# Kernel optimization log

Hardware: AMD Instinct MI355X
Metric: run time of the kernel (lower is better)

## Reference

```python
import jax, jax.numpy as jnp
import numpy as np

N = 100000      # num vertices
E = 20000       # num hyperedges
NNZ = 600000    # num incidence pairs
D = 128         # feature dim (in_features == out_features)


def _scatter_mean(src, idx, num_segments):
    # mean-reduce rows of src into num_segments buckets; empty buckets -> 0 (matches torch_scatter mean)
    s = jax.ops.segment_sum(src, idx, num_segments=num_segments)
    cnt = jax.ops.segment_sum(jnp.ones((src.shape[0], 1), src.dtype), idx, num_segments=num_segments)
    return s / jnp.maximum(cnt, 1)


def setup_inputs() -> dict:
    key = jax.random.key(0)
    k1, k2, k3, k4, k5 = jax.random.split(key, 5)
    X = jax.random.normal(k1, (N, D), dtype=jnp.float32)
    X0 = jax.random.normal(k2, (N, D), dtype=jnp.float32)
    # nn.Linear weight: [out_features, in_features], kaiming-uniform-ish scale
    W = jax.random.normal(k3, (D, D), dtype=jnp.float32) / np.float32(np.sqrt(D))
    vertex = jax.random.randint(k4, (NNZ,), 0, N)
    edges = jax.random.randint(k5, (NNZ,), 0, E)
    alpha = jnp.float32(0.1)
    beta = jnp.float32(0.5)
    return {"X": X, "vertex": vertex, "edges": edges, "alpha": alpha, "beta": beta, "X0": X0, "W": W}


def reference(X, vertex, edges, alpha, beta, X0, W):
    # vertex -> hyperedge gather + mean
    Xve = X[vertex]                                   # [NNZ, D]
    Xe = _scatter_mean(Xve, edges, E)                 # [E, D]
    # hyperedge -> vertex gather + mean
    Xev = Xe[edges]                                   # [NNZ, D]
    Xv = _scatter_mean(Xev, vertex, N)                # [N, D]
    # GCNII residual mixing (UniGNN_use_norm=False)
    Xi = (1.0 - alpha) * Xv + alpha * X0
    return (1.0 - beta) * Xi + beta * (Xi @ W.T)
```

## Files before the change

kernel.cpp:

```cpp
#include <hip/hip_runtime.h>

#define NV   100000
#define NE   20000
#define NNZP 600000
#define DIM  128
#define SE   80
#define SV   32

#define NB_E 79
#define NB_V 98
#define CAP_E 8448
#define CAP_V 6912
#define BIN_BLOCKS ((NNZP / 8 + 255) / 256)
#define G_CVT1 256
#define G_CVT2 384
#define XSPLIT4 1280000
#define EDGE_BLOCKS (NE * 16 / 256)

typedef __attribute__((ext_vector_type(8))) short short8;
typedef __attribute__((ext_vector_type(4))) float f32x4;

__device__ __forceinline__ unsigned short f2b(float f) {
    unsigned x = __float_as_uint(f);
    unsigned r = x + 0x7fffu + ((x >> 16) & 1u);
    return (unsigned short)(r >> 16);
}
__device__ __forceinline__ float blo(unsigned u) { return __uint_as_float(u << 16); }
__device__ __forceinline__ float bhi(unsigned u) { return __uint_as_float(u & 0xffff0000u); }
__device__ __forceinline__ unsigned pk2(float a, float b) {
    return (unsigned)f2b(a) | ((unsigned)f2b(b) << 16);
}

__global__ __launch_bounds__(256) void k_bin(const float4* __restrict__ X4,
                                             const float4* __restrict__ W4,
                                             const float* __restrict__ beta_p,
                                             const int4* __restrict__ vertex4,
                                             const int4* __restrict__ edges4,
                                             unsigned* __restrict__ gpos_e,
                                             unsigned* __restrict__ gpos_v,
                                             unsigned* __restrict__ ebin,
                                             unsigned* __restrict__ vbin,
                                             ushort4* __restrict__ Xb,
                                             ushort4* __restrict__ Mb) {
    const int b = blockIdx.x;
    if (b >= BIN_BLOCKS) {
        int i = (b - BIN_BLOCKS) * 256 + threadIdx.x;
        for (int g = i; g < XSPLIT4; g += G_CVT1 * 256) {
            float4 v = X4[g];
            ushort4 o; o.x = f2b(v.x); o.y = f2b(v.y); o.z = f2b(v.z); o.w = f2b(v.w);
            Xb[g] = o;
        }
        if (i < DIM * DIM / 4) {
            const float beta = *beta_p;
            const float omb  = 1.0f - beta;
            float4 v = W4[i];
            int c  = i >> 5;
            int k0 = (i & 31) * 4;
            ushort4 o;
            o.x = f2b(beta * v.x + ((k0 + 0) == c ? omb : 0.f));
            o.y = f2b(beta * v.y + ((k0 + 1) == c ? omb : 0.f));
            o.z = f2b(beta * v.z + ((k0 + 2) == c ? omb : 0.f));
            o.w = f2b(beta * v.w + ((k0 + 3) == c ? omb : 0.f));
            Mb[i] = o;
        }
        return;
    }

    __shared__ unsigned he[NB_E], hv[NB_V], be[NB_E], bv[NB_V];
    const int tid = threadIdx.x;
    if (tid < NB_E) he[tid] = 0;
    if (tid < NB_V) hv[tid] = 0;
    __syncthreads();

    const int t8 = b * 256 + tid;
    const bool ok = t8 < NNZP / 8;
    int vA[8], eA[8];
    unsigned loe[8], lov[8];
    if (ok) {
        int4 v0 = vertex4[t8 * 2], v1 = vertex4[t8 * 2 + 1];
        int4 e0 = edges4[t8 * 2],  e1 = edges4[t8 * 2 + 1];
        vA[0]=v0.x; vA[1]=v0.y; vA[2]=v0.z; vA[3]=v0.w;
        vA[4]=v1.x; vA[5]=v1.y; vA[6]=v1.z; vA[7]=v1.w;
        eA[0]=e0.x; eA[1]=e0.y; eA[2]=e0.z; eA[3]=e0.w;
        eA[4]=e1.x; eA[5]=e1.y; eA[6]=e1.z; eA[7]=e1.w;
#pragma unroll
        for (int k = 0; k < 8; ++k) {
            loe[k] = atomicAdd(&he[eA[k] >> 8], 1u);
            lov[k] = atomicAdd(&hv[vA[k] >> 10], 1u);
        }
    }
    __syncthreads();

    for (int i = tid; i < NB_E; i += 256) {
        int bin = (i + b) % NB_E;
        unsigned h = he[bin];
        be[bin] = h ? atomicAdd(&gpos_e[bin], h) : 0u;
    }
    for (int i = tid; i < NB_V; i += 256) {
        int bin = (i + b) % NB_V;
        unsigned h = hv[bin];
        bv[bin] = h ? atomicAdd(&gpos_v[bin], h) : 0u;
    }
    __syncthreads();

    if (ok) {
#pragma unroll
        for (int k = 0; k < 8; ++k) {
            unsigned e = (unsigned)eA[k], v = (unsigned)vA[k];
            unsigned binE = e >> 8, binV = v >> 10;
            unsigned pe = be[binE] + loe[k];
            if (pe < CAP_E) ebin[(size_t)binE * CAP_E + pe] = (v << 8) | (e & 255u);
            unsigned pv = bv[binV] + lov[k];
            if (pv < CAP_V) vbin[(size_t)binV * CAP_V + pv] = (e << 10) | (v & 1023u);
        }
    }
}

__global__ __launch_bounds__(256) void k_bucket(const unsigned* __restrict__ gpos_e,
                                                const unsigned* __restrict__ gpos_v,
                                                const unsigned* __restrict__ ebin,
                                                const unsigned* __restrict__ vbin,
                                                int* __restrict__ bkt_e,
                                                unsigned short* __restrict__ bkt_v,
                                                const float4* __restrict__ X4,
                                                ushort4* __restrict__ Xb) {
    const int tid = threadIdx.x;
    if (blockIdx.x >= NB_E + NB_V) {
        int i = (blockIdx.x - NB_E - NB_V) * 256 + tid;
        const int n4 = NV * 32;
        for (int g = XSPLIT4 + i; g < n4; g += G_CVT2 * 256) {
            float4 v = X4[g];
            ushort4 o; o.x = f2b(v.x); o.y = f2b(v.y); o.z = f2b(v.z); o.w = f2b(v.w);
            Xb[g] = o;
        }
        return;
    }

    __shared__ unsigned cl[1024];
    if (blockIdx.x < NB_E) {
        const int b = blockIdx.x;
        cl[tid] = 0;
        __syncthreads();
        unsigned n = gpos_e[b]; if (n > CAP_E) n = CAP_E;
        const unsigned* src = ebin + (size_t)b * CAP_E;
        for (unsigned i = tid; i < n; i += 256) {
            unsigned pk = src[i];
            unsigned el = pk & 255u;
            unsigned slot = atomicAdd(&cl[el], 1u);
            if (slot < SE - 1)
                bkt_e[(size_t)(((unsigned)b << 8) | el) * SE + 1 + slot] = (int)(pk >> 8);
        }
        __syncthreads();
        int e = (b << 8) | tid;
        if (e < NE) bkt_e[(size_t)e * SE] = (int)cl[tid];
    } else {
        const int b = blockIdx.x - NB_E;
        for (int i = tid; i < 1024; i += 256) cl[i] = 0;
        __syncthreads();
        unsigned n = gpos_v[b]; if (n > CAP_V) n = CAP_V;
        const unsigned* src = vbin + (size_t)b * CAP_V;
        for (unsigned i = tid; i < n; i += 256) {
            unsigned pk = src[i];
            unsigned vl = pk & 1023u;
            unsigned slot = atomicAdd(&cl[vl], 1u);
            unsigned v = ((unsigned)b << 10) | vl;
            if (slot < SV - 1)
                bkt_v[(size_t)v * SV + 1 + slot] = (unsigned short)(pk >> 10);
        }
        __syncthreads();
        for (int i = tid; i < 1024; i += 256) {
            int v = (b << 10) + i;
            if (v < NV) bkt_v[(size_t)v * SV] = (unsigned short)cl[i];
        }
    }
}

__global__ __launch_bounds__(256) void k_edge(const uint4* __restrict__ X4b,
                                              const int4* __restrict__ bkt4,
                                              uint4* __restrict__ Xeb4) {
    const int t  = blockIdx.x * 256 + threadIdx.x;
    const int e  = t >> 4;
    const int hl = t & 15;
    const int4* bp = bkt4 + (size_t)e * (SE / 4);
    int4 q0 = bp[0], q1 = bp[1], q2 = bp[2], q3 = bp[3], q4 = bp[4], q5 = bp[5],
         q6 = bp[6], q7 = bp[7], q8 = bp[8], q9 = bp[9], q10 = bp[10];
    unsigned c = (unsigned)q0.x; if (c > SE - 1) c = SE - 1;

    float a0=0.f,a1=0.f,a2=0.f,a3=0.f,a4=0.f,a5=0.f,a6=0.f,a7=0.f;

#define EACC(g_, w_) { a0 += (w_) * blo((g_).x); a1 += (w_) * bhi((g_).x); \
                       a2 += (w_) * blo((g_).y); a3 += (w_) * bhi((g_).y); \
                       a4 += (w_) * blo((g_).z); a5 += (w_) * bhi((g_).z); \
                       a6 += (w_) * blo((g_).w); a7 += (w_) * bhi((g_).w); }
#define EG8(qa, qb, base_) { \
        int id_[8] = {(qa).x, (qa).y, (qa).z, (qa).w, (qb).x, (qb).y, (qb).z, (qb).w}; \
        float wk_[8]; uint4 g_[8]; \
        _Pragma("unroll") \
        for (int k_ = 0; k_ < 8; ++k_) { \
            bool act_ = ((base_) + k_) < c; \
            wk_[k_] = act_ ? 1.0f : 0.0f; \
            g_[k_] = X4b[(size_t)(act_ ? (unsigned)id_[k_] : 0u) * 16 + hl]; \
        } \
        _Pragma("unroll") \
        for (int k_ = 0; k_ < 8; ++k_) EACC(g_[k_], wk_[k_]); }

    {
        int id[3] = {q0.y, q0.z, q0.w};
        float wk[3]; uint4 g[3];
#pragma unroll
        for (int k = 0; k < 3; ++k) {
            bool act = (unsigned)k < c;
            wk[k] = act ? 1.0f : 0.0f;
            g[k] = X4b[(size_t)(act ? (unsigned)id[k] : 0u) * 16 + hl];
        }
#pragma unroll
        for (int k = 0; k < 3; ++k) EACC(g[k], wk[k]);
    }
    if (c > 3)  EG8(q1, q2, 3u);
    if (c > 11) EG8(q3, q4, 11u);
    if (c > 19) EG8(q5, q6, 19u);
    if (c > 27) EG8(q7, q8, 27u);
    if (c > 35) EG8(q9, q10, 35u);
    for (unsigned j = 43; j < c; j += 8) {
        int4 qa = bp[(j + 1) >> 2];
        int4 qb = bp[((j + 1) >> 2) + 1];
        EG8(qa, qb, j);
    }
#undef EG8
#undef EACC

    const float inv = c ? 1.0f / (float)c : 1.0f;
    uint4 o;
    o.x = pk2(a0 * inv, a1 * inv);
    o.y = pk2(a2 * inv, a3 * inv);
    o.z = pk2(a4 * inv, a5 * inv);
    o.w = pk2(a6 * inv, a7 * inv);
    Xeb4[(size_t)e * 16 + hl] = o;
}

__global__ __launch_bounds__(256) void k_vf2(const uint4* __restrict__ Xeb4,
                                             const uint4* __restrict__ bktq,
                                             const float4* __restrict__ X04,
                                             const float* __restrict__ alpha_p,
                                             const unsigned short* __restrict__ Mb,
                                             float* __restrict__ out) {
    __shared__ __align__(16) unsigned sXi[16][68];

    const int tid  = threadIdx.x;
    const int wid  = tid >> 6;
    const int lane = tid & 63;
    const int q    = lane >> 4;
    const int hl   = lane & 15;
    const int vrow = wid * 4 + q;
    const int v    = blockIdx.x * 16 + vrow;

    const float alpha = *alpha_p;

    float4 x0a = X04[(size_t)v * 32 + hl * 2];
    float4 x0b = X04[(size_t)v * 32 + hl * 2 + 1];

    uint4 q0 = bktq[(size_t)v * 4];
    uint4 q1 = bktq[(size_t)v * 4 + 1];
    unsigned c = q0.x & 0xffffu; if (c > SV - 1) c = SV - 1;

    float a[8] = {0.f, 0.f, 0.f, 0.f, 0.f, 0.f, 0.f, 0.f};

#define VACC(g_, w_) { a[0] += (w_) * blo((g_).x); a[1] += (w_) * bhi((g_).x); \
                       a[2] += (w_) * blo((g_).y); a[3] += (w_) * bhi((g_).y); \
                       a[4] += (w_) * blo((g_).z); a[5] += (w_) * bhi((g_).z); \
                       a[6] += (w_) * blo((g_).w); a[7] += (w_) * bhi((g_).w); }

    {
        unsigned id[7] = { q0.x >> 16, q0.y & 0xffffu, q0.y >> 16,
                           q0.z & 0xffffu, q0.z >> 16, q0.w & 0xffffu, q0.w >> 16 };
        float wk[7]; uint4 g[7];
#pragma unroll
        for (int k = 0; k < 7; ++k) {
            bool act = (unsigned)k < c;
            wk[k] = act ? 1.0f : 0.0f;
            g[k] = Xeb4[(size_t)(act ? id[k] : 0u) * 16 + hl];
        }
#pragma unroll
        for (int k = 0; k < 7; ++k) VACC(g[k], wk[k]);
    }
    if (c > 7) {
        unsigned id[8] = { q1.x & 0xffffu, q1.x >> 16, q1.y & 0xffffu, q1.y >> 16,
                           q1.z & 0xffffu, q1.z >> 16, q1.w & 0xffffu, q1.w >> 16 };
        float wk[8]; uint4 g[8];
#pragma unroll
        for (int k = 0; k < 8; ++k) {
            bool act = (unsigned)(7 + k) < c;
            wk[k] = act ? 1.0f : 0.0f;
            g[k] = Xeb4[(size_t)(act ? id[k] : 0u) * 16 + hl];
        }
#pragma unroll
        for (int k = 0; k < 8; ++k) VACC(g[k], wk[k]);
    }
    if (c > 15) {
        uint4 q2 = bktq[(size_t)v * 4 + 2];
        uint4 q3 = bktq[(size_t)v * 4 + 3];
        unsigned id[16] = { q2.x & 0xffffu, q2.x >> 16, q2.y & 0xffffu, q2.y >> 16,
                            q2.z & 0xffffu, q2.z >> 16, q2.w & 0xffffu, q2.w >> 16,
                            q3.x & 0xffffu, q3.x >> 16, q3.y & 0xffffu, q3.y >> 16,
                            q3.z & 0xffffu, q3.z >> 16, q3.w & 0xffffu, q3.w >> 16 };
        float wk[16]; uint4 g[16];
#pragma unroll
        for (int k = 0; k < 16; ++k) {
            bool act = (unsigned)(15 + k) < c;
            wk[k] = act ? 1.0f : 0.0f;
            g[k] = Xeb4[(size_t)(act ? id[k] : 0u) * 16 + hl];
        }
#pragma unroll
        for (int k = 0; k < 16; ++k) VACC(g[k], wk[k]);
    }
#undef VACC

    const float s = (1.0f - alpha) * (c ? 1.0f / (float)c : 1.0f);
    uint4 xiw;
    xiw.x = pk2(s * a[0] + alpha * x0a.x, s * a[1] + alpha * x0a.y);
    xiw.y = pk2(s * a[2] + alpha * x0a.z, s * a[3] + alpha * x0a.w);
    xiw.z = pk2(s * a[4] + alpha * x0b.x, s * a[5] + alpha * x0b.y);
    xiw.w = pk2(s * a[6] + alpha * x0b.z, s * a[7] + alpha * x0b.w);
    *(uint4*)&sXi[vrow][hl * 4] = xiw;
    __syncthreads();

    const int lr = lane & 15;
    const int lg = lane >> 4;

    const char* ab = (const char*)&sXi[lr][0] + lg * 16;
    short8 af[4];
#pragma unroll
    for (int kt = 0; kt < 4; ++kt) af[kt] = *(const short8*)(ab + kt * 64);

#pragma unroll
    for (int ctl = 0; ctl < 2; ++ctl) {
        const int ct = wid * 2 + ctl;
        const unsigned short* Wp = Mb + (size_t)(ct * 16 + lr) * DIM + lg * 8;
        f32x4 acc = {};
#pragma unroll
        for (int kt = 0; kt < 4; ++kt) {
            short8 b = *(const short8*)(Wp + kt * 32);
            acc = __builtin_amdgcn_mfma_f32_16x16x32_bf16(af[kt], b, acc, 0, 0, 0);
        }
#pragma unroll
        for (int rg = 0; rg < 4; ++rg) {
            int row = lg * 4 + rg;
            out[(size_t)(blockIdx.x * 16 + row) * DIM + ct * 16 + lr] = acc[rg];
        }
    }
}

extern "C" void kernel_launch(void* const* d_in, const int* in_sizes, int n_in,
                              void* d_out, int out_size, void* d_ws, size_t ws_size,
                              hipStream_t stream) {
    const float* X      = (const float*)d_in[0];
    const int*   vertex = (const int*)  d_in[1];
    const int*   edges  = (const int*)  d_in[2];
    const float* alpha  = (const float*)d_in[3];
    const float* beta   = (const float*)d_in[4];
    const float* X0     = (const float*)d_in[5];
    const float* W      = (const float*)d_in[6];
    float*       out    = (float*)d_out;

    unsigned* gpos_e = (unsigned*)d_ws;
    unsigned* gpos_v = gpos_e + NB_E;
    unsigned* ebin   = (unsigned*)d_ws + 256;
    unsigned* vbin   = ebin + (size_t)NB_E * CAP_E;
    int*      bkt_e  = (int*)(vbin + (size_t)NB_V * CAP_V);
    unsigned short* bkt_v = (unsigned short*)(bkt_e + (size_t)NE * SE);
    unsigned short* Mb = bkt_v + (size_t)NV * SV;
    unsigned* Xeb = (unsigned*)(Mb + DIM * DIM);

    unsigned* Xb = (unsigned*)d_out;

    hipMemsetAsync(d_ws, 0, (size_t)(NB_E + NB_V) * sizeof(unsigned), stream);

    k_bin<<<BIN_BLOCKS + G_CVT1, 256, 0, stream>>>(
        (const float4*)X, (const float4*)W, beta,
        (const int4*)vertex, (const int4*)edges,
        gpos_e, gpos_v, ebin, vbin, (ushort4*)Xb, (ushort4*)Mb);
    k_bucket<<<NB_E + NB_V + G_CVT2, 256, 0, stream>>>(
        gpos_e, gpos_v, ebin, vbin, bkt_e, bkt_v,
        (const float4*)X, (ushort4*)Xb);
    k_edge<<<EDGE_BLOCKS, 256, 0, stream>>>((const uint4*)Xb,
                                            (const int4*)bkt_e,
                                            (uint4*)Xeb);
    k_vf2<<<NV / 16, 256, 0, stream>>>((const uint4*)Xeb, (const uint4*)bkt_v,
                                       (const float4*)X0, alpha,
                                       (const unsigned short*)Mb, out);
}
```

Before: 121.8 us.

## Make vertex-finalize kernel persistent with hoisted weights and prefetched next tile

Converts k_vf2 from one 16-vertex tile per block (6250 blocks) into a grid-stride persistent kernel with 1024 blocks. Each block loads its W fragments into registers once and reuses them across tiles, and it prefetches the next tile's X0 rows and bucket headers before the MFMA stage. The aim is to cut per-block launch and weight-reload overhead and to hide load latency. In exchange it uses more registers (launch bounds of 4 waves), adds a second barrier per tile, and may load-balance worse across CUs.

New measurement: 133.4 us. 9.5% more time.

```diff
diff --git a/kernel.cpp b/kernel.cpp
--- a/kernel.cpp
+++ b/kernel.cpp
@@ -16,6 +16,8 @@
 #define G_CVT2 384
 #define XSPLIT4 1280000
 #define EDGE_BLOCKS (NE * 16 / 256)
+#define VF2_BLOCKS 1024
+#define VF2_TILES  (NV / 16)
 
 typedef __attribute__((ext_vector_type(8))) short short8;
 typedef __attribute__((ext_vector_type(4))) float f32x4;
@@ -238,12 +240,12 @@
     Xeb4[(size_t)e * 16 + hl] = o;
 }
 
-__global__ __launch_bounds__(256) void k_vf2(const uint4* __restrict__ Xeb4,
-                                             const uint4* __restrict__ bktq,
-                                             const float4* __restrict__ X04,
-                                             const float* __restrict__ alpha_p,
-                                             const unsigned short* __restrict__ Mb,
-                                             float* __restrict__ out) {
+__global__ __launch_bounds__(256, 4) void k_vf2(const uint4* __restrict__ Xeb4,
+                                                const uint4* __restrict__ bktq,
+                                                const float4* __restrict__ X04,
+                                                const float* __restrict__ alpha_p,
+                                                const unsigned short* __restrict__ Mb,
+                                                float* __restrict__ out) {
     __shared__ __align__(16) unsigned sXi[16][68];
 
     const int tid  = threadIdx.x;
@@ -252,102 +254,125 @@
     const int q    = lane >> 4;
     const int hl   = lane & 15;
     const int vrow = wid * 4 + q;
-    const int v    = blockIdx.x * 16 + vrow;
+    const int lr   = lane & 15;
+    const int lg   = lane >> 4;
 
     const float alpha = *alpha_p;
 
+    short8 mf[2][4];
+#pragma unroll
+    for (int ctl = 0; ctl < 2; ++ctl) {
+        const unsigned short* Wp = Mb + (size_t)((wid * 2 + ctl) * 16 + lr) * DIM + lg * 8;
+#pragma unroll
+        for (int kt = 0; kt < 4; ++kt)
+            mf[ctl][kt] = *(const short8*)(Wp + kt * 32);
+    }
+
+    int tile = blockIdx.x;
+    int v = tile * 16 + vrow;
     float4 x0a = X04[(size_t)v * 32 + hl * 2];
     float4 x0b = X04[(size_t)v * 32 + hl * 2 + 1];
-
     uint4 q0 = bktq[(size_t)v * 4];
     uint4 q1 = bktq[(size_t)v * 4 + 1];
-    unsigned c = q0.x & 0xffffu; if (c > SV - 1) c = SV - 1;
-
-    float a[8] = {0.f, 0.f, 0.f, 0.f, 0.f, 0.f, 0.f, 0.f};
 
 #define VACC(g_, w_) { a[0] += (w_) * blo((g_).x); a[1] += (w_) * bhi((g_).x); \
                        a[2] += (w_) * blo((g_).y); a[3] += (w_) * bhi((g_).y); \
                        a[4] += (w_) * blo((g_).z); a[5] += (w_) * bhi((g_).z); \
                        a[6] += (w_) * blo((g_).w); a[7] += (w_) * bhi((g_).w); }
 
-    {
-        unsigned id[7] = { q0.x >> 16, q0.y & 0xffffu, q0.y >> 16,
-                           q0.z & 0xffffu, q0.z >> 16, q0.w & 0xffffu, q0.w >> 16 };
-        float wk[7]; uint4 g[7];
-#pragma unroll
-        for (int k = 0; k < 7; ++k) {
-            bool act = (unsigned)k < c;
-            wk[k] = act ? 1.0f : 0.0f;
-            g[k] = Xeb4[(size_t)(act ? id[k] : 0u) * 16 + hl];
-        }
-#pragma unroll
-        for (int k = 0; k < 7; ++k) VACC(g[k], wk[k]);
-    }
-    if (c > 7) {
-        unsigned id[8] = { q1.x & 0xffffu, q1.x >> 16, q1.y & 0xffffu, q1.y >> 16,
-                           q1.z & 0xffffu, q1.z >> 16, q1.w & 0xffffu, q1.w >> 16 };
-        float wk[8]; uint4 g[8];
-#pragma unroll
-        for (int k = 0; k < 8; ++k) {
-            bool act = (unsigned)(7 + k) < c;
-            wk[k] = act ? 1.0f : 0.0f;
-            g[k] = Xeb4[(size_t)(act ? id[k] : 0u) * 16 + hl];
-        }
-#pragma unroll
-        for (int k = 0; k < 8; ++k) VACC(g[k], wk[k]);
-    }
-    if (c > 15) {
-        uint4 q2 = bktq[(size_t)v * 4 + 2];
-        uint4 q3 = bktq[(size_t)v * 4 + 3];
-        unsigned id[16] = { q2.x & 0xffffu, q2.x >> 16, q2.y & 0xffffu, q2.y >> 16,
-                            q2.z & 0xffffu, q2.z >> 16, q2.w & 0xffffu, q2.w >> 16,
-                            q3.x & 0xffffu, q3.x >> 16, q3.y & 0xffffu, q3.y >> 16,
-                            q3.z & 0xffffu, q3.z >> 16, q3.w & 0xffffu, q3.w >> 16 };
-        float wk[16]; uint4 g[16];
-#pragma unroll
-        for (int k = 0; k < 16; ++k) {
-            bool act = (unsigned)(15 + k) < c;
-            wk[k] = act ? 1.0f : 0.0f;
-            g[k] = Xeb4[(size_t)(act ? id[k] : 0u) * 16 + hl];
-        }
-#pragma unroll
-        for (int k = 0; k < 16; ++k) VACC(g[k], wk[k]);
+    while (true) {
+        unsigned c = q0.x & 0xffffu; if (c > SV - 1) c = SV - 1;
+        float a[8] = {0.f, 0.f, 0.f, 0.f, 0.f, 0.f, 0.f, 0.f};
+
+        {
+            unsigned id[7] = { q0.x >> 16, q0.y & 0xffffu, q0.y >> 16,
+                               q0.z & 0xffffu, q0.z >> 16, q0.w & 0xffffu, q0.w >> 16 };
+            float wk[7]; uint4 g[7];
+#pragma unroll
+            for (int k = 0; k < 7; ++k) {
+                bool act = (unsigned)k < c;
+                wk[k] = act ? 1.0f : 0.0f;
+                g[k] = Xeb4[(size_t)(act ? id[k] : 0u) * 16 + hl];
+            }
+#pragma unroll
+            for (int k = 0; k < 7; ++k) VACC(g[k], wk[k]);
+        }
+        if (c > 7) {
+            unsigned id[8] = { q1.x & 0xffffu, q1.x >> 16, q1.y & 0xffffu, q1.y >> 16,
+                               q1.z & 0xffffu, q1.z >> 16, q1.w & 0xffffu, q1.w >> 16 };
+            float wk[8]; uint4 g[8];
+#pragma unroll
+            for (int k = 0; k < 8; ++k) {
+                bool act = (unsigned)(7 + k) < c;
+                wk[k] = act ? 1.0f : 0.0f;
+                g[k] = Xeb4[(size_t)(act ? id[k] : 0u) * 16 + hl];
+            }
+#pragma unroll
+            for (int k = 0; k < 8; ++k) VACC(g[k], wk[k]);
+        }
+        if (c > 15) {
+            uint4 q2 = bktq[(size_t)v * 4 + 2];
+            uint4 q3 = bktq[(size_t)v * 4 + 3];
+            unsigned id[16] = { q2.x & 0xffffu, q2.x >> 16, q2.y & 0xffffu, q2.y >> 16,
+                                q2.z & 0xffffu, q2.z >> 16, q2.w & 0xffffu, q2.w >> 16,
+                                q3.x & 0xffffu, q3.x >> 16, q3.y & 0xffffu, q3.y >> 16,
+                                q3.z & 0xffffu, q3.z >> 16, q3.w & 0xffffu, q3.w >> 16 };
+            float wk[16]; uint4 g[16];
+#pragma unroll
+            for (int k = 0; k < 16; ++k) {
+                bool act = (unsigned)(15 + k) < c;
+                wk[k] = act ? 1.0f : 0.0f;
+                g[k] = Xeb4[(size_t)(act ? id[k] : 0u) * 16 + hl];
+            }
+#pragma unroll
+            for (int k = 0; k < 16; ++k) VACC(g[k], wk[k]);
+        }
+
+        const float s = (1.0f - alpha) * (c ? 1.0f / (float)c : 1.0f);
+        uint4 xiw;
+        xiw.x = pk2(s * a[0] + alpha * x0a.x, s * a[1] + alpha * x0a.y);
+        xiw.y = pk2(s * a[2] + alpha * x0a.z, s * a[3] + alpha * x0a.w);
+        xiw.z = pk2(s * a[4] + alpha * x0b.x, s * a[5] + alpha * x0b.y);
+        xiw.w = pk2(s * a[6] + alpha * x0b.z, s * a[7] + alpha * x0b.w);
+        *(uint4*)&sXi[vrow][hl * 4] = xiw;
+
+        const int ntile = tile + VF2_BLOCKS;
+        const bool more = ntile < VF2_TILES;
+        const int nv = ntile * 16 + vrow;
+        float4 nx0a, nx0b; uint4 nq0, nq1;
+        if (more) {
+            nx0a = X04[(size_t)nv * 32 + hl * 2];
+            nx0b = X04[(size_t)nv * 32 + hl * 2 + 1];
+            nq0 = bktq[(size_t)nv * 4];
+            nq1 = bktq[(size_t)nv * 4 + 1];
+        }
+        __syncthreads();
+
+        const char* ab = (const char*)&sXi[lr][0] + lg * 16;
+        short8 af[4];
+#pragma unroll
+        for (int kt = 0; kt < 4; ++kt) af[kt] = *(const short8*)(ab + kt * 64);
+
+#pragma unroll
+        for (int ctl = 0; ctl < 2; ++ctl) {
+            const int ct = wid * 2 + ctl;
+            f32x4 acc = {};
+#pragma unroll
+            for (int kt = 0; kt < 4; ++kt)
+                acc = __builtin_amdgcn_mfma_f32_16x16x32_bf16(af[kt], mf[ctl][kt], acc, 0, 0, 0);
+#pragma unroll
+            for (int rg = 0; rg < 4; ++rg) {
+                int row = lg * 4 + rg;
+                out[(size_t)(tile * 16 + row) * DIM + ct * 16 + lr] = acc[rg];
+            }
+        }
+        __syncthreads();
+
+        if (!more) break;
+        tile = ntile; v = nv;
+        x0a = nx0a; x0b = nx0b; q0 = nq0; q1 = nq1;
     }
 #undef VACC
-
-    const float s = (1.0f - alpha) * (c ? 1.0f / (float)c : 1.0f);
-    uint4 xiw;
-    xiw.x = pk2(s * a[0] + alpha * x0a.x, s * a[1] + alpha * x0a.y);
-    xiw.y = pk2(s * a[2] + alpha * x0a.z, s * a[3] + alpha * x0a.w);
-    xiw.z = pk2(s * a[4] + alpha * x0b.x, s * a[5] + alpha * x0b.y);
-    xiw.w = pk2(s * a[6] + alpha * x0b.z, s * a[7] + alpha * x0b.w);
-    *(uint4*)&sXi[vrow][hl * 4] = xiw;
-    __syncthreads();
-
-    const int lr = lane & 15;
-    const int lg = lane >> 4;
-
-    const char* ab = (const char*)&sXi[lr][0] + lg * 16;
-    short8 af[4];
-#pragma unroll
-    for (int kt = 0; kt < 4; ++kt) af[kt] = *(const short8*)(ab + kt * 64);
-
-#pragma unroll
-    for (int ctl = 0; ctl < 2; ++ctl) {
-        const int ct = wid * 2 + ctl;
-        const unsigned short* Wp = Mb + (size_t)(ct * 16 + lr) * DIM + lg * 8;
-        f32x4 acc = {};
-#pragma unroll
-        for (int kt = 0; kt < 4; ++kt) {
-            short8 b = *(const short8*)(Wp + kt * 32);
-            acc = __builtin_amdgcn_mfma_f32_16x16x32_bf16(af[kt], b, acc, 0, 0, 0);
-        }
-#pragma unroll
-        for (int rg = 0; rg < 4; ++rg) {
-            int row = lg * 4 + rg;
-            out[(size_t)(blockIdx.x * 16 + row) * DIM + ct * 16 + lr] = acc[rg];
-        }
-    }
 }
 
 extern "C" void kernel_launch(void* const* d_in, const int* in_sizes, int n_in,
@@ -385,7 +410,7 @@
     k_edge<<<EDGE_BLOCKS, 256, 0, stream>>>((const uint4*)Xb,
                                             (const int4*)bkt_e,
                                             (uint4*)Xeb);
-    k_vf2<<<NV / 16, 256, 0, stream>>>((const uint4*)Xeb, (const uint4*)bkt_v,
-                                       (const float4*)X0, alpha,
-                                       (const unsigned short*)Mb, out);
-}
+    k_vf2<<<VF2_BLOCKS, 256, 0, stream>>>((const uint4*)Xeb, (const uint4*)bkt_v,
+                                          (const float4*)X0, alpha,
+                                          (const unsigned short*)Mb, out);
+}
```

## Double-buffer edge gathers and process two vertex rows per thread in k_vf2

Applied to the files above, without the earlier changes.

In k_edge, the gather loads for each group of 8 incidences are split from their accumulation and alternated between two register buffers, so the next group's loads are issued before the previous group's FMAs. In k_vf2, each block now handles 32 vertices instead of 16. Each thread interleaves the first gathers of two vertices to raise memory-level parallelism, and reuses the W tiles loaded for the MFMA across two row tiles. Register pressure rises in both kernels and the k_vf2 grid is halved, which may lower occupancy.

New measurement: 122.4 us. No clear change (+0.5%).

```diff
diff --git a/kernel.cpp b/kernel.cpp
--- a/kernel.cpp
+++ b/kernel.cpp
@@ -16,6 +16,7 @@
 #define G_CVT2 384
 #define XSPLIT4 1280000
 #define EDGE_BLOCKS (NE * 16 / 256)
+#define VF2_BLOCKS (NV / 32)
 
 typedef __attribute__((ext_vector_type(8))) short short8;
 typedef __attribute__((ext_vector_type(4))) float f32x4;
@@ -192,41 +193,48 @@
                        a2 += (w_) * blo((g_).y); a3 += (w_) * bhi((g_).y); \
                        a4 += (w_) * blo((g_).z); a5 += (w_) * bhi((g_).z); \
                        a6 += (w_) * blo((g_).w); a7 += (w_) * bhi((g_).w); }
-#define EG8(qa, qb, base_) { \
+#define LD8(gb_, wb_, qa, qb, base_) { \
         int id_[8] = {(qa).x, (qa).y, (qa).z, (qa).w, (qb).x, (qb).y, (qb).z, (qb).w}; \
-        float wk_[8]; uint4 g_[8]; \
         _Pragma("unroll") \
         for (int k_ = 0; k_ < 8; ++k_) { \
             bool act_ = ((base_) + k_) < c; \
-            wk_[k_] = act_ ? 1.0f : 0.0f; \
-            g_[k_] = X4b[(size_t)(act_ ? (unsigned)id_[k_] : 0u) * 16 + hl]; \
-        } \
+            wb_[k_] = act_ ? 1.0f : 0.0f; \
+            gb_[k_] = X4b[(size_t)(act_ ? (unsigned)id_[k_] : 0u) * 16 + hl]; \
+        } }
+#define FM8(gb_, wb_) { \
         _Pragma("unroll") \
-        for (int k_ = 0; k_ < 8; ++k_) EACC(g_[k_], wk_[k_]); }
-
-    {
+        for (int k_ = 0; k_ < 8; ++k_) EACC(gb_[k_], wb_[k_]); }
+
+    float w0[3]; uint4 g0[3];
+#pragma unroll
+    for (int k = 0; k < 3; ++k) {
         int id[3] = {q0.y, q0.z, q0.w};
-        float wk[3]; uint4 g[3];
-#pragma unroll
-        for (int k = 0; k < 3; ++k) {
-            bool act = (unsigned)k < c;
-            wk[k] = act ? 1.0f : 0.0f;
-            g[k] = X4b[(size_t)(act ? (unsigned)id[k] : 0u) * 16 + hl];
-        }
-#pragma unroll
-        for (int k = 0; k < 3; ++k) EACC(g[k], wk[k]);
-    }
-    if (c > 3)  EG8(q1, q2, 3u);
-    if (c > 11) EG8(q3, q4, 11u);
-    if (c > 19) EG8(q5, q6, 19u);
-    if (c > 27) EG8(q7, q8, 27u);
-    if (c > 35) EG8(q9, q10, 35u);
+        bool act = (unsigned)k < c;
+        w0[k] = act ? 1.0f : 0.0f;
+        g0[k] = X4b[(size_t)(act ? (unsigned)id[k] : 0u) * 16 + hl];
+    }
+
+    float wX[8], wY[8]; uint4 gX[8], gY[8];
+    if (c > 3)  LD8(gX, wX, q1, q2, 3u);
+#pragma unroll
+    for (int k = 0; k < 3; ++k) EACC(g0[k], w0[k]);
+    if (c > 11) LD8(gY, wY, q3, q4, 11u);
+    if (c > 3)  FM8(gX, wX);
+    if (c > 19) LD8(gX, wX, q5, q6, 19u);
+    if (c > 11) FM8(gY, wY);
+    if (c > 27) LD8(gY, wY, q7, q8, 27u);
+    if (c > 19) FM8(gX, wX);
+    if (c > 35) LD8(gX, wX, q9, q10, 35u);
+    if (c > 27) FM8(gY, wY);
+    if (c > 35) FM8(gX, wX);
     for (unsigned j = 43; j < c; j += 8) {
         int4 qa = bp[(j + 1) >> 2];
         int4 qb = bp[((j + 1) >> 2) + 1];
-        EG8(qa, qb, j);
-    }
-#undef EG8
+        LD8(gY, wY, qa, qb, j);
+        FM8(gY, wY);
+    }
+#undef LD8
+#undef FM8
 #undef EACC
 
     const float inv = c ? 1.0f / (float)c : 1.0f;
@@ -244,7 +252,7 @@
                                              const float* __restrict__ alpha_p,
                                              const unsigned short* __restrict__ Mb,
                                              float* __restrict__ out) {
-    __shared__ __align__(16) unsigned sXi[16][68];
+    __shared__ __align__(16) unsigned sXi[32][68];
 
     const int tid  = threadIdx.x;
     const int wid  = tid >> 6;
@@ -252,53 +260,73 @@
     const int q    = lane >> 4;
     const int hl   = lane & 15;
     const int vrow = wid * 4 + q;
-    const int v    = blockIdx.x * 16 + vrow;
+    const int lr   = lane & 15;
+    const int lg   = lane >> 4;
 
     const float alpha = *alpha_p;
-
-    float4 x0a = X04[(size_t)v * 32 + hl * 2];
-    float4 x0b = X04[(size_t)v * 32 + hl * 2 + 1];
-
-    uint4 q0 = bktq[(size_t)v * 4];
-    uint4 q1 = bktq[(size_t)v * 4 + 1];
-    unsigned c = q0.x & 0xffffu; if (c > SV - 1) c = SV - 1;
-
-    float a[8] = {0.f, 0.f, 0.f, 0.f, 0.f, 0.f, 0.f, 0.f};
-
-#define VACC(g_, w_) { a[0] += (w_) * blo((g_).x); a[1] += (w_) * bhi((g_).x); \
-                       a[2] += (w_) * blo((g_).y); a[3] += (w_) * bhi((g_).y); \
-                       a[4] += (w_) * blo((g_).z); a[5] += (w_) * bhi((g_).z); \
-                       a[6] += (w_) * blo((g_).w); a[7] += (w_) * bhi((g_).w); }
+    const int v0 = blockIdx.x * 32 + vrow;
+    const int v1 = v0 + 16;
+
+    uint4 q0a = bktq[(size_t)v0 * 4];
+    uint4 q1a = bktq[(size_t)v0 * 4 + 1];
+    uint4 q0b = bktq[(size_t)v1 * 4];
+    uint4 q1b = bktq[(size_t)v1 * 4 + 1];
+    float4 x0a0 = X04[(size_t)v0 * 32 + hl * 2];
+    float4 x0b0 = X04[(size_t)v0 * 32 + hl * 2 + 1];
+    float4 x0a1 = X04[(size_t)v1 * 32 + hl * 2];
+    float4 x0b1 = X04[(size_t)v1 * 32 + hl * 2 + 1];
+
+    unsigned ca = q0a.x & 0xffffu; if (ca > SV - 1) ca = SV - 1;
+    unsigned cb = q0b.x & 0xffffu; if (cb > SV - 1) cb = SV - 1;
+
+    float aA[8] = {0.f,0.f,0.f,0.f,0.f,0.f,0.f,0.f};
+    float aB[8] = {0.f,0.f,0.f,0.f,0.f,0.f,0.f,0.f};
+
+#define VACC(acc_, g_, w_) { acc_[0] += (w_) * blo((g_).x); acc_[1] += (w_) * bhi((g_).x); \
+                             acc_[2] += (w_) * blo((g_).y); acc_[3] += (w_) * bhi((g_).y); \
+                             acc_[4] += (w_) * blo((g_).z); acc_[5] += (w_) * bhi((g_).z); \
+                             acc_[6] += (w_) * blo((g_).w); acc_[7] += (w_) * bhi((g_).w); }
 
     {
-        unsigned id[7] = { q0.x >> 16, q0.y & 0xffffu, q0.y >> 16,
-                           q0.z & 0xffffu, q0.z >> 16, q0.w & 0xffffu, q0.w >> 16 };
-        float wk[7]; uint4 g[7];
+        unsigned idA[7] = { q0a.x >> 16, q0a.y & 0xffffu, q0a.y >> 16,
+                            q0a.z & 0xffffu, q0a.z >> 16, q0a.w & 0xffffu, q0a.w >> 16 };
+        unsigned idB[7] = { q0b.x >> 16, q0b.y & 0xffffu, q0b.y >> 16,
+                            q0b.z & 0xffffu, q0b.z >> 16, q0b.w & 0xffffu, q0b.w >> 16 };
+        float wA[7], wB[7]; uint4 gA[7], gB[7];
 #pragma unroll
         for (int k = 0; k < 7; ++k) {
-            bool act = (unsigned)k < c;
+            bool act = (unsigned)k < ca;
+            wA[k] = act ? 1.0f : 0.0f;
+            gA[k] = Xeb4[(size_t)(act ? idA[k] : 0u) * 16 + hl];
+        }
+#pragma unroll
+        for (int k = 0; k < 7; ++k) {
+            bool act = (unsigned)k < cb;
+            wB[k] = act ? 1.0f : 0.0f;
+            gB[k] = Xeb4[(size_t)(act ? idB[k] : 0u) * 16 + hl];
+        }
+#pragma unroll
+        for (int k = 0; k < 7; ++k) VACC(aA, gA[k], wA[k]);
+#pragma unroll
+        for (int k = 0; k < 7; ++k) VACC(aB, gB[k], wB[k]);
+    }
+
+    if (ca > 7) {
+        unsigned id[8] = { q1a.x & 0xffffu, q1a.x >> 16, q1a.y & 0xffffu, q1a.y >> 16,
+                           q1a.z & 0xffffu, q1a.z >> 16, q1a.w & 0xffffu, q1a.w >> 16 };
+        float wk[8]; uint4 g[8];
+#pragma unroll
+        for (int k = 0; k < 8; ++k) {
+            bool act = (unsigned)(7 + k) < ca;
             wk[k] = act ? 1.0f : 0.0f;
             g[k] = Xeb4[(size_t)(act ? id[k] : 0u) * 16 + hl];
         }
 #pragma unroll
-        for (int k = 0; k < 7; ++k) VACC(g[k], wk[k]);
-    }
-    if (c > 7) {
-        unsigned id[8] = { q1.x & 0xffffu, q1.x >> 16, q1.y & 0xffffu, q1.y >> 16,
-                           q1.z & 0xffffu, q1.z >> 16, q1.w & 0xffffu, q1.w >> 16 };
-        float wk[8]; uint4 g[8];
-#pragma unroll
-        for (int k = 0; k < 8; ++k) {
-            bool act = (unsigned)(7 + k) < c;
-            wk[k] = act ? 1.0f : 0.0f;
-            g[k] = Xeb4[(size_t)(act ? id[k] : 0u) * 16 + hl];
-        }
-#pragma unroll
-        for (int k = 0; k < 8; ++k) VACC(g[k], wk[k]);
-    }
-    if (c > 15) {
-        uint4 q2 = bktq[(size_t)v * 4 + 2];
-        uint4 q3 = bktq[(size_t)v * 4 + 3];
+        for (int k = 0; k < 8; ++k) VACC(aA, g[k], wk[k]);
+    }
+    if (ca > 15) {
+        uint4 q2 = bktq[(size_t)v0 * 4 + 2];
+        uint4 q3 = bktq[(size_t)v0 * 4 + 3];
         unsigned id[16] = { q2.x & 0xffffu, q2.x >> 16, q2.y & 0xffffu, q2.y >> 16,
                             q2.z & 0xffffu, q2.z >> 16, q2.w & 0xffffu, q2.w >> 16,
                             q3.x & 0xffffu, q3.x >> 16, q3.y & 0xffffu, q3.y >> 16,
@@ -306,46 +334,90 @@
         float wk[16]; uint4 g[16];
 #pragma unroll
         for (int k = 0; k < 16; ++k) {
-            bool act = (unsigned)(15 + k) < c;
+            bool act = (unsigned)(15 + k) < ca;
             wk[k] = act ? 1.0f : 0.0f;
             g[k] = Xeb4[(size_t)(act ? id[k] : 0u) * 16 + hl];
         }
 #pragma unroll
-        for (int k = 0; k < 16; ++k) VACC(g[k], wk[k]);
+        for (int k = 0; k < 16; ++k) VACC(aA, g[k], wk[k]);
+    }
+
+    if (cb > 7) {
+        unsigned id[8] = { q1b.x & 0xffffu, q1b.x >> 16, q1b.y & 0xffffu, q1b.y >> 16,
+                           q1b.z & 0xffffu, q1b.z >> 16, q1b.w & 0xffffu, q1b.w >> 16 };
+        float wk[8]; uint4 g[8];
+#pragma unroll
+        for (int k = 0; k < 8; ++k) {
+            bool act = (unsigned)(7 + k) < cb;
+            wk[k] = act ? 1.0f : 0.0f;
+            g[k] = Xeb4[(size_t)(act ? id[k] : 0u) * 16 + hl];
+        }
+#pragma unroll
+        for (int k = 0; k < 8; ++k) VACC(aB, g[k], wk[k]);
+    }
+    if (cb > 15) {
+        uint4 q2 = bktq[(size_t)v1 * 4 + 2];
+        uint4 q3 = bktq[(size_t)v1 * 4 + 3];
+        unsigned id[16] = { q2.x & 0xffffu, q2.x >> 16, q2.y & 0xffffu, q2.y >> 16,
+                            q2.z & 0xffffu, q2.z >> 16, q2.w & 0xffffu, q2.w >> 16,
+                            q3.x & 0xffffu, q3.x >> 16, q3.y & 0xffffu, q3.y >> 16,
+                            q3.z & 0xffffu, q3.z >> 16, q3.w & 0xffffu, q3.w >> 16 };
+        float wk[16]; uint4 g[16];
+#pragma unroll
+        for (int k = 0; k < 16; ++k) {
+            bool act = (unsigned)(15 + k) < cb;
+            wk[k] = act ? 1.0f : 0.0f;
+            g[k] = Xeb4[(size_t)(act ? id[k] : 0u) * 16 + hl];
+        }
+#pragma unroll
+        for (int k = 0; k < 16; ++k) VACC(aB, g[k], wk[k]);
     }
 #undef VACC
 
-    const float s = (1.0f - alpha) * (c ? 1.0f / (float)c : 1.0f);
-    uint4 xiw;
-    xiw.x = pk2(s * a[0] + alpha * x0a.x, s * a[1] + alpha * x0a.y);
-    xiw.y = pk2(s * a[2] + alpha * x0a.z, s * a[3] + alpha * x0a.w);
-    xiw.z = pk2(s * a[4] + alpha * x0b.x, s * a[5] + alpha * x0b.y);
-    xiw.w = pk2(s * a[6] + alpha * x0b.z, s * a[7] + alpha * x0b.w);
-    *(uint4*)&sXi[vrow][hl * 4] = xiw;
+    {
+        const float s = (1.0f - alpha) * (ca ? 1.0f / (float)ca : 1.0f);
+        uint4 xiw;
+        xiw.x = pk2(s * aA[0] + alpha * x0a0.x, s * aA[1] + alpha * x0a0.y);
+        xiw.y = pk2(s * aA[2] + alpha * x0a0.z, s * aA[3] + alpha * x0a0.w);
+        xiw.z = pk2(s * aA[4] + alpha * x0b0.x, s * aA[5] + alpha * x0b0.y);
+        xiw.w = pk2(s * aA[6] + alpha * x0b0.z, s * aA[7] + alpha * x0b0.w);
+        *(uint4*)&sXi[vrow][hl * 4] = xiw;
+    }
+    {
+        const float s = (1.0f - alpha) * (cb ? 1.0f / (float)cb : 1.0f);
+        uint4 xiw;
+        xiw.x = pk2(s * aB[0] + alpha * x0a1.x, s * aB[1] + alpha * x0a1.y);
+        xiw.y = pk2(s * aB[2] + alpha * x0a1.z, s * aB[3] + alpha * x0a1.w);
+        xiw.z = pk2(s * aB[4] + alpha * x0b1.x, s * aB[5] + alpha * x0b1.y);
+        xiw.w = pk2(s * aB[6] + alpha * x0b1.z, s * aB[7] + alpha * x0b1.w);
+        *(uint4*)&sXi[vrow + 16][hl * 4] = xiw;
+    }
+
     __syncthreads();
 
-    const int lr = lane & 15;
-    const int lg = lane >> 4;
-
-    const char* ab = (const char*)&sXi[lr][0] + lg * 16;
-    short8 af[4];
-#pragma unroll
-    for (int kt = 0; kt < 4; ++kt) af[kt] = *(const short8*)(ab + kt * 64);
-
-#pragma unroll
-    for (int ctl = 0; ctl < 2; ++ctl) {
-        const int ct = wid * 2 + ctl;
-        const unsigned short* Wp = Mb + (size_t)(ct * 16 + lr) * DIM + lg * 8;
-        f32x4 acc = {};
-#pragma unroll
-        for (int kt = 0; kt < 4; ++kt) {
-            short8 b = *(const short8*)(Wp + kt * 32);
-            acc = __builtin_amdgcn_mfma_f32_16x16x32_bf16(af[kt], b, acc, 0, 0, 0);
-        }
-#pragma unroll
-        for (int rg = 0; rg < 4; ++rg) {
-            int row = lg * 4 + rg;
-            out[(size_t)(blockIdx.x * 16 + row) * DIM + ct * 16 + lr] = acc[rg];
+    const size_t obase = (size_t)blockIdx.x * 32 * DIM;
+#pragma unroll
+    for (int rt = 0; rt < 2; ++rt) {
+        const char* ab = (const char*)&sXi[rt * 16 + lr][0] + lg * 16;
+        short8 af[4];
+#pragma unroll
+        for (int kt = 0; kt < 4; ++kt) af[kt] = *(const short8*)(ab + kt * 64);
+
+#pragma unroll
+        for (int ctl = 0; ctl < 2; ++ctl) {
+            const int ct = wid * 2 + ctl;
+            const unsigned short* Wp = Mb + (size_t)(ct * 16 + lr) * DIM + lg * 8;
+            f32x4 acc = {};
+#pragma unroll
+            for (int kt = 0; kt < 4; ++kt) {
+                short8 b = *(const short8*)(Wp + kt * 32);
+                acc = __builtin_amdgcn_mfma_f32_16x16x32_bf16(af[kt], b, acc, 0, 0, 0);
+            }
+#pragma unroll
+            for (int rg = 0; rg < 4; ++rg) {
+                int row = rt * 16 + lg * 4 + rg;
+                out[obase + (size_t)row * DIM + ct * 16 + lr] = acc[rg];
+            }
         }
     }
 }
@@ -385,7 +457,7 @@
     k_edge<<<EDGE_BLOCKS, 256, 0, stream>>>((const uint4*)Xb,
                                             (const int4*)bkt_e,
                                             (uint4*)Xeb);
-    k_vf2<<<NV / 16, 256, 0, stream>>>((const uint4*)Xeb, (const uint4*)bkt_v,
-                                       (const float4*)X0, alpha,
-                                       (const unsigned short*)Mb, out);
-}
+    k_vf2<<<VF2_BLOCKS, 256, 0, stream>>>((const uint4*)Xeb, (const uint4*)bkt_v,
+                                          (const float4*)X0, alpha,
+                                          (const unsigned short*)Mb, out);
+}
```
